# Performance work log

Measured on AMD Instinct MI355X. Metric: run time of the kernel, lower is better.

## Reference

```python
import jax, jax.numpy as jnp
import numpy as np

N = 30000          # num nodes
DEG = 32           # rrwp pairs per node (includes self-loop offset 0)
N_EDGE_OFF = 16    # edge offsets per node -> E = N*16
RW = 16            # rw_steps
DPE = 32           # dim_pe
DEMB = 128         # dim_emb
DIN = 64           # GT_gnn.dim_inner
NODE_FEAT = 16     # num_linear_emb_node
BN_EPS = 1e-5


def _lin(key, fan_in, fan_out):
    k1, k2 = jax.random.split(key)
    s = 1.0 / np.sqrt(fan_in)
    W = jax.random.uniform(k1, (fan_in, fan_out), minval=-s, maxval=s, dtype=jnp.float32)
    b = jax.random.uniform(k2, (fan_out,), minval=-s, maxval=s, dtype=jnp.float32)
    return W, b


def setup_inputs() -> dict:
    rng = np.random.default_rng(0)
    # rrwp_idx: for each node i, pairs (i, (i+d) mod N) for DEG distinct offsets incl. 0
    offs = np.concatenate([np.zeros(1, np.int64),
                           rng.choice(np.arange(1, N, dtype=np.int64), size=DEG - 1, replace=False)])
    rows = np.tile(np.arange(N, dtype=np.int64), DEG)
    cols = (rows + np.repeat(offs, N)) % N
    rrwp_idx = jnp.asarray(np.stack([rows, cols]))              # [2, N*DEG], unique pairs, superset of edges+self-loops
    e_offs = offs[1:1 + N_EDGE_OFF]                              # edges are a subset of rrwp pairs (non-zero offsets)
    erows = np.tile(np.arange(N, dtype=np.int64), N_EDGE_OFF)
    ecols = (erows + np.repeat(e_offs, N)) % N
    edge_index = jnp.asarray(np.stack([erows, ecols]))           # [2, N*16]

    key = jax.random.key(0)
    ks = jax.random.split(key, 16)
    x = jax.random.normal(ks[0], (N, NODE_FEAT), jnp.float32)
    edge_attr = jax.random.normal(ks[1], (N * N_EDGE_OFF,), jnp.float32)
    rrwp = jax.random.uniform(ks[2], (N, RW), dtype=jnp.float32)
    rrwp_val = jax.random.uniform(ks[3], (N * DEG, RW), dtype=jnp.float32)

    Wh, bh = _lin(ks[4], NODE_FEAT, DEMB - DPE)   # embedding_h (linear)
    We, be = _lin(ks[5], 1, DIN)                  # embedding_e (linear on scalar edge attr)
    Wn, bn_ = _lin(ks[6], RW, DPE)                # fc_node
    pe_w1, pe_b1 = _lin(ks[7], DPE, 2 * DPE)      # pe_encoder (n_layers=2)
    pe_w2, pe_b2 = _lin(ks[8], 2 * DPE, DPE)
    Wedge, bedge = _lin(ks[9], RW, DIN)           # fc_edge
    ee_w1, ee_b1 = _lin(ks[10], DIN, 2 * DIN)     # ee_encoder (n_layers=2)
    ee_w2, ee_b2 = _lin(ks[11], 2 * DIN, DIN)
    gamma = jnp.ones((DIN,), jnp.float32)         # bn weight
    beta = jnp.zeros((DIN,), jnp.float32)         # bn bias
    return dict(x=x, edge_attr=edge_attr, rrwp=rrwp, rrwp_val=rrwp_val,
                edge_index=edge_index, rrwp_idx=rrwp_idx,
                Wh=Wh, bh=bh, We=We, be=be, Wn=Wn, bn_=bn_,
                pe_w1=pe_w1, pe_b1=pe_b1, pe_w2=pe_w2, pe_b2=pe_b2,
                Wedge=Wedge, bedge=bedge, ee_w1=ee_w1, ee_b1=ee_b1,
                ee_w2=ee_w2, ee_b2=ee_b2, gamma=gamma, beta=beta)


def reference(x, edge_attr, rrwp, rrwp_val, edge_index, rrwp_idx,
              Wh, bh, We, be, Wn, bn_, pe_w1, pe_b1, pe_w2, pe_b2,
              Wedge, bedge, ee_w1, ee_b1, ee_w2, ee_b2, gamma, beta):
    relu = jax.nn.relu
    # node features: embedding_h + RRWP node PE (fc_node -> MLP)
    h = x @ Wh + bh                                   # [N, DEMB-DPE]
    pe = rrwp @ Wn + bn_                              # [N, DPE]
    pe = relu(pe @ pe_w1 + pe_b1)
    pe = relu(pe @ pe_w2 + pe_b2)
    x_out = jnp.concatenate([h, pe], axis=1)          # [N, DEMB]

    # edge features
    eattr = edge_attr[:, None] @ We + be              # [E, DIN]  (embedding_e on scalar attr)
    rv = rrwp_val @ Wedge + bedge                     # [E_rrwp, DIN] (fc_edge)
    rv = relu(rv @ ee_w1 + ee_b1)                     # ee_encoder
    rv = relu(rv @ ee_w2 + ee_b2)

    # coalesce(add): rrwp_idx is a unique superset of edges + self-loops, so the
    # coalesced index set equals sorted(rrwp_idx); edge attrs scatter-add onto it.
    # Self-loop attrs are zero-filled (fill_value=0.0) -> adding them is a no-op.
    n = x.shape[0]
    keys = rrwp_idx[0] * n + rrwp_idx[1]              # linearized (row, col) keys
    order = jnp.argsort(keys)
    skeys = keys[order]
    sidx = rrwp_idx[:, order]                         # coalesced out_idx [2, E_rrwp]
    sval = rv[order]
    ekeys = edge_index[0] * n + edge_index[1]
    pos = jnp.searchsorted(skeys, ekeys)              # position of each edge within rrwp pattern
    out_val = sval.at[pos].add(eattr)

    # BatchNorm1d (training-mode batch statistics, biased var)
    mu = jnp.mean(out_val, axis=0)
    var = jnp.mean((out_val - mu) ** 2, axis=0)
    out_val = (out_val - mu) * jax.lax.rsqrt(var + BN_EPS) * gamma + beta
    return x_out, sidx, out_val
```

## Files before the change

### kernel.cpp

```cpp
#include <hip/hip_runtime.h>
#include <cstdint>
#include <cstddef>

#define NN 30000
#define DEG 32
#define NEO 16
#define NROWS (NN * DEG)

typedef __attribute__((ext_vector_type(8))) short bf16x8;
typedef __attribute__((ext_vector_type(4))) float f32x4;
typedef __attribute__((ext_vector_type(4))) unsigned u32x4;

__device__ __forceinline__ short f2bf(float f) {
    union { float f; unsigned u; } v; v.f = f;
    unsigned r = (v.u + 0x7FFFu + ((v.u >> 16) & 1u)) >> 16;
    return (short)r;
}

__device__ __forceinline__ unsigned pktr(float a, float b) {
    unsigned ua = __builtin_bit_cast(unsigned, a);
    unsigned ub = __builtin_bit_cast(unsigned, b);
    return (ua >> 16) | (ub & 0xFFFF0000u);
}

__device__ __forceinline__ bf16x8 pack2(f32x4 x, f32x4 y) {
    u32x4 d;
    d[0] = pktr(x[0], x[1]); d[1] = pktr(x[2], x[3]);
    d[2] = pktr(y[0], y[1]); d[3] = pktr(y[2], y[3]);
    return __builtin_bit_cast(bf16x8, d);
}

__device__ __forceinline__ f32x4 relu4(f32x4 v) {
    f32x4 r;
    r[0] = fmaxf(v[0], 0.f); r[1] = fmaxf(v[1], 0.f);
    r[2] = fmaxf(v[2], 0.f); r[3] = fmaxf(v[3], 0.f);
    return r;
}

__global__ __launch_bounds__(64) void k_wprep(
    const float* __restrict__ Wedge, const float* __restrict__ bedge,
    const float* __restrict__ w1, const float* __restrict__ w2,
    unsigned short* __restrict__ wfrag, float* __restrict__ gstats)
{
    int f = blockIdx.x;
    int l = threadIdx.x;
    if (f == 0) { gstats[l] = 0.0f; gstats[l + 64] = 0.0f; }
    int lhi = l >> 4, llo = l & 15;
    unsigned short out[8];
    #pragma unroll
    for (int i = 0; i < 8; ++i) {
        int k = lhi * 8 + i;
        float val;
        if (f < 4) {
            int col = f * 16 + llo;
            if (k < 16)       val = Wedge[k * 64 + col];
            else if (k == 16) val = bedge[col];
            else              val = 0.0f;
        } else if (f < 20) {
            int idx = f - 4; int nt = idx >> 1, s = idx & 1;
            int kap = 16 * (2 * s + (i >> 2)) + 4 * lhi + (i & 3);
            val = w1[kap * 128 + nt * 16 + llo];
        } else {
            int idx = f - 20; int t = idx >> 2, s = idx & 3;
            int kap = 16 * (2 * s + (i >> 2)) + 4 * lhi + (i & 3);
            val = w2[kap * 64 + t * 16 + llo];
        }
        out[i] = (unsigned short)f2bf(val);
    }
    #pragma unroll
    for (int i = 0; i < 8; ++i) wfrag[((size_t)f * 64 + l) * 8 + i] = out[i];
}

__global__ __launch_bounds__(256) void k_xout(
    const float* __restrict__ x, const float* __restrict__ rrwp,
    const float* __restrict__ Wh, const float* __restrict__ bh,
    const float* __restrict__ Wn, const float* __restrict__ bnb,
    const float* __restrict__ pw1, const float* __restrict__ pb1,
    const float* __restrict__ pw2, const float* __restrict__ pb2,
    float* __restrict__ out)
{
    int r = blockIdx.x * 256 + threadIdx.x;
    if (r >= NN) return;
    float xv[16], rv[16];
    {
        const float4* p = (const float4*)(x + (size_t)r * 16);
        float4 a = p[0], b = p[1], c = p[2], d = p[3];
        xv[0]=a.x; xv[1]=a.y; xv[2]=a.z; xv[3]=a.w;
        xv[4]=b.x; xv[5]=b.y; xv[6]=b.z; xv[7]=b.w;
        xv[8]=c.x; xv[9]=c.y; xv[10]=c.z; xv[11]=c.w;
        xv[12]=d.x; xv[13]=d.y; xv[14]=d.z; xv[15]=d.w;
    }
    {
        const float4* p = (const float4*)(rrwp + (size_t)r * 16);
        float4 a = p[0], b = p[1], c = p[2], d = p[3];
        rv[0]=a.x; rv[1]=a.y; rv[2]=a.z; rv[3]=a.w;
        rv[4]=b.x; rv[5]=b.y; rv[6]=b.z; rv[7]=b.w;
        rv[8]=c.x; rv[9]=c.y; rv[10]=c.z; rv[11]=c.w;
        rv[12]=d.x; rv[13]=d.y; rv[14]=d.z; rv[15]=d.w;
    }
    float* orow = out + (size_t)r * 128;
    #pragma unroll
    for (int j = 0; j < 96; ++j) {
        float a = bh[j];
        #pragma unroll
        for (int i = 0; i < 16; ++i) a = fmaf(xv[i], Wh[i * 96 + j], a);
        orow[j] = a;
    }
    float p0[32];
    #pragma unroll
    for (int j = 0; j < 32; ++j) {
        float a = bnb[j];
        #pragma unroll
        for (int i = 0; i < 16; ++i) a = fmaf(rv[i], Wn[i * 32 + j], a);
        p0[j] = a;
    }
    float p1[64];
    #pragma unroll
    for (int j = 0; j < 64; ++j) {
        float a = pb1[j];
        #pragma unroll
        for (int i = 0; i < 32; ++i) a = fmaf(p0[i], pw1[i * 64 + j], a);
        p1[j] = fmaxf(a, 0.0f);
    }
    #pragma unroll
    for (int j = 0; j < 32; ++j) {
        float a = pb2[j];
        #pragma unroll
        for (int i = 0; i < 64; ++i) a = fmaf(p1[i], pw2[i * 32 + j], a);
        orow[96 + j] = fmaxf(a, 0.0f);
    }
}

__global__ __launch_bounds__(256) void k_rank(
    const int* __restrict__ cols, int* __restrict__ sortpos,
    float* __restrict__ sidx0, float* __restrict__ sidx1)
{
    int i = blockIdx.x * 256 + threadIdx.x;
    int d = i / NN;
    int r = i - d * NN;
    int c = cols[i];
    int rank = 0;
    #pragma unroll
    for (int d2 = 0; d2 < DEG; ++d2) {
        int c2 = cols[d2 * NN + r];
        rank += (c2 < c) ? 1 : 0;
    }
    int p = r * DEG + rank;
    sortpos[i] = p;
    sidx0[p] = (float)r;
    sidx1[p] = (float)c;
}

template<int PHASE>
__global__ __launch_bounds__(256, 2) void k_mlp(
    const float* __restrict__ rrwp_val, const float* __restrict__ edge_attr,
    const unsigned short* __restrict__ wfrag,
    const float* __restrict__ b1, const float* __restrict__ b2,
    const float* __restrict__ We, const float* __restrict__ be,
    const int* __restrict__ sortpos,
    const float* __restrict__ gamma, const float* __restrict__ beta,
    float* __restrict__ out_val, float* __restrict__ gsum, float* __restrict__ gsq)
{
    __shared__ __align__(16) unsigned short lwf3[16 * 64 * 8];
    __shared__ __align__(16) float s_b2c[128];
    __shared__ float s_sum[64];
    __shared__ float s_sq[64];

    int tid = threadIdx.x;
    int w = tid >> 6, l = tid & 63;
    int lhi = l >> 4, llo = l & 15;

    {
        const float4* s = (const float4*)(wfrag + (size_t)20 * 64 * 8);
        float4* dst = (float4*)lwf3;
        #pragma unroll
        for (int k = 0; k < 4; ++k) dst[tid + k * 256] = s[tid + k * 256];
    }
    if (tid < 32) {
        int lh = tid >> 3, nt = tid & 7;
        ((f32x4*)s_b2c)[tid] = *(const f32x4*)(b1 + nt * 16 + 4 * lh);
    }
    if (PHASE == 0) {
        if (tid < 64) { s_sum[tid] = 0.0f; s_sq[tid] = 0.0f; }
    }
    __syncthreads();

    const unsigned short* wl3 = lwf3 + (size_t)l * 8;
    #define WF3(f) (*(const bf16x8*)(wl3 + (f) * 512))

    bf16x8 wf[20];
    #pragma unroll
    for (int f = 0; f < 20; ++f)
        wf[f] = *(const bf16x8*)(wfrag + ((size_t)f * 64 + l) * 8);

    float bias3[4], weS[4], beS[4], bnsc[4], bnsh[4];
    #pragma unroll
    for (int t = 0; t < 4; ++t) {
        int fidx = t * 16 + llo;
        bias3[t] = b2[fidx];
        weS[t] = We[fidx];
        beS[t] = be[fidx];
        if (PHASE == 1) {
            const float inv = 1.0f / (float)NROWS;
            float mu  = gsum[fidx] * inv;
            float var = gsq[fidx] * inv - mu * mu;
            float sc  = rsqrtf(var + 1e-5f) * gamma[fidx];
            bnsc[t] = sc;
            bnsh[t] = beta[fidx] - mu * sc;
        } else { bnsc[t] = 0.0f; bnsh[t] = 0.0f; }
    }
    float ssum[4] = {0.f, 0.f, 0.f, 0.f};
    float ssq[4]  = {0.f, 0.f, 0.f, 0.f};

    #pragma unroll 1
    for (int it = 0; it < 8; ++it) {
        int tb = blockIdx.x * 512 + it * 64 + w * 16;

        const float4* src = (const float4*)(rrwp_val + (size_t)(tb + llo) * 16 + (size_t)(lhi & 1) * 8);
        float4 u0 = src[0], u1 = src[1];
        unsigned d0 = pktr(u0.x, u0.y), d1 = pktr(u0.z, u0.w);
        unsigned d2 = pktr(u1.x, u1.y), d3 = pktr(u1.z, u1.w);
        if (lhi >= 2) { d0 = (lhi == 2) ? 0x3F80u : 0u; d1 = 0u; d2 = 0u; d3 = 0u; }
        u32x4 a1d = {d0, d1, d2, d3};
        bf16x8 a1 = __builtin_bit_cast(bf16x8, a1d);

        f32x4 acc1[4];
        #pragma unroll
        for (int t = 0; t < 4; ++t) {
            f32x4 z = {0.f, 0.f, 0.f, 0.f};
            acc1[t] = __builtin_amdgcn_mfma_f32_16x16x32_bf16(wf[t], a1, z, 0, 0, 0);
        }

        bf16x8 a2[2];
        a2[0] = pack2(acc1[0], acc1[1]);
        a2[1] = pack2(acc1[2], acc1[3]);
        bf16x8 a3[4];
        #pragma unroll
        for (int h = 0; h < 2; ++h) {
            f32x4 acc2[4];
            #pragma unroll
            for (int q = 0; q < 4; ++q) {
                int nt = h * 4 + q;
                f32x4 c2 = ((const f32x4*)s_b2c)[lhi * 8 + nt];
                acc2[q] = __builtin_amdgcn_mfma_f32_16x16x32_bf16(wf[4 + nt * 2 + 0], a2[0], c2, 0, 0, 0);
                acc2[q] = __builtin_amdgcn_mfma_f32_16x16x32_bf16(wf[4 + nt * 2 + 1], a2[1], acc2[q], 0, 0, 0);
            }
            a3[2 * h]     = pack2(relu4(acc2[0]), relu4(acc2[1]));
            a3[2 * h + 1] = pack2(relu4(acc2[2]), relu4(acc2[3]));
        }

        f32x4 acc3[4];
        #pragma unroll
        for (int t = 0; t < 4; ++t) {
            f32x4 c3 = {bias3[t], bias3[t], bias3[t], bias3[t]};
            acc3[t] = __builtin_amdgcn_mfma_f32_16x16x32_bf16(a3[0], WF3(t * 4 + 0), c3, 0, 0, 0);
            acc3[t] = __builtin_amdgcn_mfma_f32_16x16x32_bf16(a3[1], WF3(t * 4 + 1), acc3[t], 0, 0, 0);
            acc3[t] = __builtin_amdgcn_mfma_f32_16x16x32_bf16(a3[2], WF3(t * 4 + 2), acc3[t], 0, 0, 0);
            acc3[t] = __builtin_amdgcn_mfma_f32_16x16x32_bf16(a3[3], WF3(t * 4 + 3), acc3[t], 0, 0, 0);
        }

        int d = tb / NN;
        int rbase = tb - d * NN;
        bool edged = (d >= 1 && d <= NEO);
        float ev[4]; int pp[4];
        #pragma unroll
        for (int r = 0; r < 4; ++r) {
            int row = lhi * 4 + r;
            ev[r] = edged ? edge_attr[(size_t)(d - 1) * NN + rbase + row] : 0.0f;
            pp[r] = (PHASE == 1) ? sortpos[tb + row] : 0;
        }
        #pragma unroll
        for (int t = 0; t < 4; ++t)
            #pragma unroll
            for (int r = 0; r < 4; ++r) {
                float v = fmaxf(acc3[t][r], 0.0f);
                if (edged) v = fmaf(ev[r], weS[t], v + beS[t]);
                if (PHASE == 0) {
                    ssum[t] += v;
                    ssq[t]   = fmaf(v, v, ssq[t]);
                } else {
                    out_val[(size_t)pp[r] * 64 + t * 16 + llo] = fmaf(v, bnsc[t], bnsh[t]);
                }
            }
    }
    #undef WF3

    if (PHASE == 0) {
        __syncthreads();
        #pragma unroll
        for (int t = 0; t < 4; ++t) {
            float s = ssum[t], q = ssq[t];
            s += __shfl_xor(s, 16); q += __shfl_xor(q, 16);
            s += __shfl_xor(s, 32); q += __shfl_xor(q, 32);
            if (lhi == 0) { atomicAdd(&s_sum[t * 16 + llo], s); atomicAdd(&s_sq[t * 16 + llo], q); }
        }
        __syncthreads();
        if (tid < 64)       atomicAdd(&gsum[tid], s_sum[tid]);
        else if (tid < 128) atomicAdd(&gsq[tid - 64], s_sq[tid - 64]);
    }
}

extern "C" void kernel_launch(void* const* d_in, const int* in_sizes, int n_in,
                              void* d_out, int out_size, void* d_ws, size_t ws_size,
                              hipStream_t stream)
{
    const float* x         = (const float*)d_in[0];
    const float* edge_attr = (const float*)d_in[1];
    const float* rrwp      = (const float*)d_in[2];
    const float* rrwp_val  = (const float*)d_in[3];
    const int*   rrwp_idx  = (const int*)d_in[5];
    const float* Wh    = (const float*)d_in[6];
    const float* bh    = (const float*)d_in[7];
    const float* We    = (const float*)d_in[8];
    const float* be    = (const float*)d_in[9];
    const float* Wn    = (const float*)d_in[10];
    const float* bnb   = (const float*)d_in[11];
    const float* pw1   = (const float*)d_in[12];
    const float* pb1   = (const float*)d_in[13];
    const float* pw2   = (const float*)d_in[14];
    const float* pb2   = (const float*)d_in[15];
    const float* Wedge = (const float*)d_in[16];
    const float* bedge = (const float*)d_in[17];
    const float* ew1   = (const float*)d_in[18];
    const float* eb1   = (const float*)d_in[19];
    const float* ew2   = (const float*)d_in[20];
    const float* eb2   = (const float*)d_in[21];
    const float* gamma = (const float*)d_in[22];
    const float* beta  = (const float*)d_in[23];

    float* out       = (float*)d_out;
    float* out_xout  = out;
    float* out_sidx0 = out + (size_t)NN * 128;
    float* out_sidx1 = out_sidx0 + NROWS;
    float* out_val   = out_sidx1 + NROWS;

    float* ws    = (float*)d_ws;
    float* gsum  = ws;
    float* gsq   = ws + 64;
    int*   sortpos = (int*)(ws + 256);
    unsigned short* wfrag = (unsigned short*)(ws + 256 + NROWS);

    const int* cols = rrwp_idx + NROWS;

    k_wprep<<<36, 64, 0, stream>>>(Wedge, bedge, ew1, ew2, wfrag, gsum);
    k_xout<<<(NN + 255) / 256, 256, 0, stream>>>(x, rrwp, Wh, bh, Wn, bnb, pw1, pb1, pw2, pb2, out_xout);
    k_rank<<<NROWS / 256, 256, 0, stream>>>(cols, sortpos, out_sidx0, out_sidx1);
    k_mlp<0><<<1875, 256, 0, stream>>>(rrwp_val, edge_attr, wfrag, eb1, eb2, We, be,
                                       sortpos, gamma, beta, out_val, gsum, gsq);
    k_mlp<1><<<1875, 256, 0, stream>>>(rrwp_val, edge_attr, wfrag, eb1, eb2, We, be,
                                       sortpos, gamma, beta, out_val, gsum, gsq);
}
```

Baseline: 224.9 us.

## Rank per node with one thread and move layer-2 weights to LDS

k_rank now runs one thread per node. Each thread loads all 32 column indices once, ranks them in registers, and writes the sidx0 row as vectorised float4 stores, instead of one thread per pair re-reading 32 columns. In k_mlp the 16 layer-2 weight fragments move from per-lane registers into shared memory alongside the layer-3 fragments, which cuts VGPR pressure at the cost of more LDS reads per iteration. The rank change reduces redundant global reads but launches far fewer threads (about 118 blocks), so parallelism drops and the sidx1 stores become scattered per thread.

```diff
diff --git a/kernel.cpp b/kernel.cpp
--- a/kernel.cpp
+++ b/kernel.cpp
@@ -135,20 +135,23 @@
     const int* __restrict__ cols, int* __restrict__ sortpos,
     float* __restrict__ sidx0, float* __restrict__ sidx1)
 {
-    int i = blockIdx.x * 256 + threadIdx.x;
-    int d = i / NN;
-    int r = i - d * NN;
-    int c = cols[i];
-    int rank = 0;
-    #pragma unroll
-    for (int d2 = 0; d2 < DEG; ++d2) {
-        int c2 = cols[d2 * NN + r];
-        rank += (c2 < c) ? 1 : 0;
-    }
-    int p = r * DEG + rank;
-    sortpos[i] = p;
-    sidx0[p] = (float)r;
-    sidx1[p] = (float)c;
+    int r = blockIdx.x * 256 + threadIdx.x;
+    if (r >= NN) return;
+    int c[DEG];
+    #pragma unroll
+    for (int d = 0; d < DEG; ++d) c[d] = cols[(size_t)d * NN + r];
+    float4 rsplat = { (float)r, (float)r, (float)r, (float)r };
+    float4* s0 = (float4*)(sidx0 + (size_t)r * DEG);
+    #pragma unroll
+    for (int k = 0; k < 8; ++k) s0[k] = rsplat;
+    #pragma unroll 4
+    for (int d = 0; d < DEG; ++d) {
+        int rank = 0;
+        #pragma unroll
+        for (int k = 0; k < DEG; ++k) rank += (c[k] < c[d]) ? 1 : 0;
+        sortpos[(size_t)d * NN + r] = r * DEG + rank;
+        sidx1[(size_t)r * DEG + rank] = (float)c[d];
+    }
 }
 
 template<int PHASE>
@@ -161,7 +164,7 @@
     const float* __restrict__ gamma, const float* __restrict__ beta,
     float* __restrict__ out_val, float* __restrict__ gsum, float* __restrict__ gsq)
 {
-    __shared__ __align__(16) unsigned short lwf3[16 * 64 * 8];
+    __shared__ __align__(16) unsigned short lwf[32 * 64 * 8];
     __shared__ __align__(16) float s_b2c[128];
     __shared__ float s_sum[64];
     __shared__ float s_sq[64];
@@ -171,10 +174,10 @@
     int lhi = l >> 4, llo = l & 15;
 
     {
-        const float4* s = (const float4*)(wfrag + (size_t)20 * 64 * 8);
-        float4* dst = (float4*)lwf3;
-        #pragma unroll
-        for (int k = 0; k < 4; ++k) dst[tid + k * 256] = s[tid + k * 256];
+        const float4* s = (const float4*)(wfrag + (size_t)4 * 64 * 8);
+        float4* dst = (float4*)lwf;
+        #pragma unroll
+        for (int k = 0; k < 8; ++k) dst[tid + k * 256] = s[tid + k * 256];
     }
     if (tid < 32) {
         int lh = tid >> 3, nt = tid & 7;
@@ -185,13 +188,13 @@
     }
     __syncthreads();
 
-    const unsigned short* wl3 = lwf3 + (size_t)l * 8;
-    #define WF3(f) (*(const bf16x8*)(wl3 + (f) * 512))
-
-    bf16x8 wf[20];
-    #pragma unroll
-    for (int f = 0; f < 20; ++f)
-        wf[f] = *(const bf16x8*)(wfrag + ((size_t)f * 64 + l) * 8);
+    const unsigned short* wl = lwf + (size_t)l * 8;
+    #define WFL(fl) (*(const bf16x8*)(wl + (fl) * 512))
+
+    bf16x8 wf1[4];
+    #pragma unroll
+    for (int f = 0; f < 4; ++f)
+        wf1[f] = *(const bf16x8*)(wfrag + ((size_t)f * 64 + l) * 8);
 
     float bias3[4], weS[4], beS[4], bnsc[4], bnsh[4];
     #pragma unroll
@@ -228,7 +231,7 @@
         #pragma unroll
         for (int t = 0; t < 4; ++t) {
             f32x4 z = {0.f, 0.f, 0.f, 0.f};
-            acc1[t] = __builtin_amdgcn_mfma_f32_16x16x32_bf16(wf[t], a1, z, 0, 0, 0);
+            acc1[t] = __builtin_amdgcn_mfma_f32_16x16x32_bf16(wf1[t], a1, z, 0, 0, 0);
         }
 
         bf16x8 a2[2];
@@ -242,8 +245,8 @@
             for (int q = 0; q < 4; ++q) {
                 int nt = h * 4 + q;
                 f32x4 c2 = ((const f32x4*)s_b2c)[lhi * 8 + nt];
-                acc2[q] = __builtin_amdgcn_mfma_f32_16x16x32_bf16(wf[4 + nt * 2 + 0], a2[0], c2, 0, 0, 0);
-                acc2[q] = __builtin_amdgcn_mfma_f32_16x16x32_bf16(wf[4 + nt * 2 + 1], a2[1], acc2[q], 0, 0, 0);
+                acc2[q] = __builtin_amdgcn_mfma_f32_16x16x32_bf16(WFL(nt * 2 + 0), a2[0], c2, 0, 0, 0);
+                acc2[q] = __builtin_amdgcn_mfma_f32_16x16x32_bf16(WFL(nt * 2 + 1), a2[1], acc2[q], 0, 0, 0);
             }
             a3[2 * h]     = pack2(relu4(acc2[0]), relu4(acc2[1]));
             a3[2 * h + 1] = pack2(relu4(acc2[2]), relu4(acc2[3]));
@@ -253,10 +256,10 @@
         #pragma unroll
         for (int t = 0; t < 4; ++t) {
             f32x4 c3 = {bias3[t], bias3[t], bias3[t], bias3[t]};
-            acc3[t] = __builtin_amdgcn_mfma_f32_16x16x32_bf16(a3[0], WF3(t * 4 + 0), c3, 0, 0, 0);
-            acc3[t] = __builtin_amdgcn_mfma_f32_16x16x32_bf16(a3[1], WF3(t * 4 + 1), acc3[t], 0, 0, 0);
-            acc3[t] = __builtin_amdgcn_mfma_f32_16x16x32_bf16(a3[2], WF3(t * 4 + 2), acc3[t], 0, 0, 0);
-            acc3[t] = __builtin_amdgcn_mfma_f32_16x16x32_bf16(a3[3], WF3(t * 4 + 3), acc3[t], 0, 0, 0);
+            acc3[t] = __builtin_amdgcn_mfma_f32_16x16x32_bf16(a3[0], WFL(16 + t * 4 + 0), c3, 0, 0, 0);
+            acc3[t] = __builtin_amdgcn_mfma_f32_16x16x32_bf16(a3[1], WFL(16 + t * 4 + 1), acc3[t], 0, 0, 0);
+            acc3[t] = __builtin_amdgcn_mfma_f32_16x16x32_bf16(a3[2], WFL(16 + t * 4 + 2), acc3[t], 0, 0, 0);
+            acc3[t] = __builtin_amdgcn_mfma_f32_16x16x32_bf16(a3[3], WFL(16 + t * 4 + 3), acc3[t], 0, 0, 0);
         }
 
         int d = tb / NN;
@@ -283,7 +286,7 @@
                 }
             }
     }
-    #undef WF3
+    #undef WFL
 
     if (PHASE == 0) {
         __syncthreads();
@@ -344,7 +347,7 @@
 
     k_wprep<<<36, 64, 0, stream>>>(Wedge, bedge, ew1, ew2, wfrag, gsum);
     k_xout<<<(NN + 255) / 256, 256, 0, stream>>>(x, rrwp, Wh, bh, Wn, bnb, pw1, pb1, pw2, pb2, out_xout);
-    k_rank<<<NROWS / 256, 256, 0, stream>>>(cols, sortpos, out_sidx0, out_sidx1);
+    k_rank<<<(NN + 255) / 256, 256, 0, stream>>>(cols, sortpos, out_sidx0, out_sidx1);
     k_mlp<0><<<1875, 256, 0, stream>>>(rrwp_val, edge_attr, wfrag, eb1, eb2, We, be,
                                        sortpos, gamma, beta, out_val, gsum, gsq);
     k_mlp<1><<<1875, 256, 0, stream>>>(rrwp_val, edge_attr, wfrag, eb1, eb2, We, be,
```

Result: faster. 210.2 us, median of 2 (-6.5%).
